# Optimization experiments

Hardware: AMD Instinct MI355X
Metric: run time of the kernel (lower is better)

The kernel has to match this reference:

```python
import jax, jax.numpy as jnp
import numpy as np

B, S, D, H = 4, 2048, 512, 8
E = D // H  # d_head = 64

def setup_inputs() -> dict:
    key = jax.random.key(0)
    ks = jax.random.split(key, 10)
    s_in = (1.0 / np.sqrt(D))
    x  = jax.random.normal(ks[0], (B, S, D), dtype=jnp.float32)
    Wq = jax.random.normal(ks[1], (H, D, E), dtype=jnp.float32) * s_in
    bq = jax.random.normal(ks[2], (H, E), dtype=jnp.float32) * 0.01
    Wk = jax.random.normal(ks[3], (H, D, E), dtype=jnp.float32) * s_in
    bk = jax.random.normal(ks[4], (H, E), dtype=jnp.float32) * 0.01
    Wv = jax.random.normal(ks[5], (H, D, E), dtype=jnp.float32) * s_in
    bv = jax.random.normal(ks[6], (H, E), dtype=jnp.float32) * 0.01
    Wo = jax.random.normal(ks[7], (D, D), dtype=jnp.float32) * s_in
    bo = jax.random.normal(ks[8], (D,), dtype=jnp.float32) * 0.01
    return {"x": x, "Wq": Wq, "bq": bq, "Wk": Wk, "bk": bk,
            "Wv": Wv, "bv": bv, "Wo": Wo, "bo": bo}

def reference(x, Wq, bq, Wk, bk, Wv, bv, Wo, bo):
    B_, S_, D_ = x.shape
    # per-head projections (batched over head axis h)
    q = jnp.einsum('bsd,hde->bhse', x, Wq) + bq[None, :, None, :]
    k = jnp.einsum('bsd,hde->bhse', x, Wk) + bk[None, :, None, :]
    v = jnp.einsum('bsd,hde->bhse', x, Wv) + bv[None, :, None, :]
    # NOTE: original scales by d_model**-0.5 (full D), not d_head**-0.5
    scale = jnp.asarray(D_, x.dtype) ** -0.5
    scores = jnp.einsum('bhse,bhte->bhst', q, k) * scale  # [B,H,S,S]
    causal = jnp.tril(jnp.ones((S_, S_), dtype=bool))
    scores = jnp.where(causal[None, None], scores, -jnp.inf)
    attn = jax.nn.softmax(scores, axis=-1)
    out = jnp.einsum('bhst,bhte->bhse', attn, v)  # [B,H,S,E]
    # concat heads along feature dim (head-major), matching torch.cat
    out = out.transpose(0, 2, 1, 3).reshape(B_, S_, D_)
    return out @ Wo + bo  # final projection; dropout never applied in source
```

## Files before the change

kernel.cpp:

```cpp
#include <hip/hip_runtime.h>

typedef unsigned short u16;
typedef __bf16 bf16x8 __attribute__((ext_vector_type(8)));
typedef short s16x4 __attribute__((ext_vector_type(4)));
typedef short s16x8 __attribute__((ext_vector_type(8)));
typedef float f32x4 __attribute__((ext_vector_type(4)));

#define BB 4
#define SS 2048
#define DD 512
#define HH 8
#define EE 64
#define MM 8192
#define BHSE (BB*HH*SS*EE)

__device__ __forceinline__ float b2f(u16 u) {
    return __uint_as_float(((unsigned int)u) << 16);
}
__device__ __forceinline__ u16 f2b(float f) {
    unsigned int v = __float_as_uint(f);
    v += 0x7fffu + ((v >> 16) & 1u);
    return (u16)(v >> 16);
}
__device__ __forceinline__ float loadE(const void* p, size_t idx, int isbf16) {
    return isbf16 ? b2f(((const u16*)p)[idx]) : ((const float*)p)[idx];
}
__device__ __forceinline__ f32x4 mfma16x16x16_bf16(s16x4 a, s16x4 b, f32x4 c) {
    return __builtin_amdgcn_mfma_f32_16x16x16bf16_1k(a, b, c, 0, 0, 0);
}

__device__ __forceinline__ int detect_bf16(const u16* x) {
    int sane = 0;
    for (int i = 0; i < 128; ++i) {
        float a = fabsf(b2f(x[2 * i]));
        if (a == 0.f || (a > 1e-4f && a < 100.f)) ++sane;
    }
    return sane >= 96;
}

__global__ __launch_bounds__(256) void transpose_weights(
    const void* __restrict__ Wq, const void* __restrict__ Wk,
    const void* __restrict__ Wv, const void* __restrict__ Wo,
    const u16* __restrict__ xin,
    u16* __restrict__ WT, u16* __restrict__ WoT, int* __restrict__ flag)
{
    const int isbf16 = detect_bf16(xin);
    if (blockIdx.x == 0 && threadIdx.x == 0) *flag = isbf16;

    const int j = blockIdx.x;
    const int job = j >> 6;
    const int t = j & 63;
    const void* src; u16* dst; int src_ld, dst_ld;
    if (job < 3) {
        const void* W = (job == 0) ? Wq : ((job == 1) ? Wk : Wv);
        int h = t >> 3, kt = t & 7;
        size_t off = (size_t)h * DD * EE + (size_t)kt * 64 * EE;
        src = isbf16 ? (const void*)(((const u16*)W) + off)
                     : (const void*)(((const float*)W) + off);
        src_ld = EE;
        dst = WT + (size_t)job * 512 * 512 + (size_t)(h * 64) * 512 + kt * 64;
        dst_ld = 512;
    } else {
        int a = t >> 3, b = t & 7;
        size_t off = (size_t)(a * 64) * 512 + b * 64;
        src = isbf16 ? (const void*)(((const u16*)Wo) + off)
                     : (const void*)(((const float*)Wo) + off);
        src_ld = 512;
        dst = WoT + (size_t)(b * 64) * 512 + a * 64;
        dst_ld = 512;
    }
    __shared__ __align__(16) u16 Ts[64 * 72];
    const int tid = threadIdx.x;
#pragma unroll
    for (int it = 0; it < 2; ++it) {
        int idx = it * 256 + tid;
        int r = idx >> 3, c = (idx & 7) << 3;
#pragma unroll
        for (int k = 0; k < 8; ++k) {
            float v = loadE(src, (size_t)r * src_ld + c + k, isbf16);
            Ts[(c + k) * 72 + r] = f2b(v);
        }
    }
    __syncthreads();
#pragma unroll
    for (int it = 0; it < 2; ++it) {
        int idx = it * 256 + tid;
        int r = idx >> 3, c = (idx & 7) << 3;
        *(bf16x8*)(dst + (size_t)r * dst_ld + c) = *(const bf16x8*)&Ts[r * 72 + c];
    }
}

__global__ __launch_bounds__(256) void gemm_qkv(
    const void* __restrict__ X, const u16* __restrict__ WT,
    const void* __restrict__ bq, const void* __restrict__ bk,
    const void* __restrict__ bv, u16* __restrict__ qkv,
    const int* __restrict__ flag)
{
    const float SCALE = 0.04419417382415922f;
    const int isbf16 = *flag;
    const int m0 = blockIdx.x * 64;
    const int n0 = blockIdx.y * 64;
    const int tid = threadIdx.x;
    const int wave = tid >> 6, lane = tid & 63;
    const int lq = lane & 15, quad = lane >> 4;
    __shared__ __align__(16) u16 As[64 * 72];
    __shared__ __align__(16) u16 Bs[64 * 72];
    f32x4 acc[4] = {};
    for (int k0 = 0; k0 < 512; k0 += 64) {
        __syncthreads();
#pragma unroll
        for (int it = 0; it < 2; ++it) {
            int idx = it * 256 + tid;
            int r = idx >> 3, c = (idx & 7) << 3;
            size_t eoff = (size_t)(m0 + r) * 512 + k0 + c;
            if (isbf16) {
                *(bf16x8*)&As[r * 72 + c] = *(const bf16x8*)(((const u16*)X) + eoff);
            } else {
                const float* Xf = ((const float*)X) + eoff;
                float4 f0 = *(const float4*)Xf;
                float4 f1 = *(const float4*)(Xf + 4);
                u16 tmp[8] = { f2b(f0.x), f2b(f0.y), f2b(f0.z), f2b(f0.w),
                               f2b(f1.x), f2b(f1.y), f2b(f1.z), f2b(f1.w) };
                *(bf16x8*)&As[r * 72 + c] = *(const bf16x8*)tmp;
            }
            *(bf16x8*)&Bs[r * 72 + c] = *(const bf16x8*)(WT + (size_t)(n0 + r) * 512 + k0 + c);
        }
        __syncthreads();
        const u16* Arow = &As[(16 * wave + lq) * 72];
        bf16x8 a0 = *(const bf16x8*)(Arow + quad * 8);
        bf16x8 a1 = *(const bf16x8*)(Arow + 32 + quad * 8);
#pragma unroll
        for (int nt = 0; nt < 4; ++nt) {
            const u16* Brow = &Bs[(nt * 16 + lq) * 72];
            bf16x8 b0 = *(const bf16x8*)(Brow + quad * 8);
            bf16x8 b1 = *(const bf16x8*)(Brow + 32 + quad * 8);
            acc[nt] = __builtin_amdgcn_mfma_f32_16x16x32_bf16(a0, b0, acc[nt], 0, 0, 0);
            acc[nt] = __builtin_amdgcn_mfma_f32_16x16x32_bf16(a1, b1, acc[nt], 0, 0, 0);
        }
    }
#pragma unroll
    for (int nt = 0; nt < 4; ++nt) {
#pragma unroll
        for (int r = 0; r < 4; ++r) {
            int m = m0 + 16 * wave + quad * 4 + r;
            int n = n0 + nt * 16 + lq;
            int proj = n >> 9, nn = n & 511;
            const void* bias = (proj == 0) ? bq : ((proj == 1) ? bk : bv);
            float v = acc[nt][r] + loadE(bias, nn, isbf16);
            if (proj == 0) v *= SCALE;
            int b = m >> 11, s = m & 2047, h = nn >> 6, e = nn & 63;
            qkv[(size_t)proj * BHSE + (((size_t)(b * HH + h) * SS + s) * EE + e)] = f2b(v);
        }
    }
}

struct Stage { uint4 k0, k1, va, vb; };

__device__ __forceinline__ void stage_load(Stage& st, const u16* Kh, const u16* Vh,
                                           int t0, int tid) {
    int r = tid >> 3, c = (tid & 7) * 8;
    st.k0 = *(const uint4*)(Kh + (size_t)(t0 + r) * 64 + c);
    st.k1 = *(const uint4*)(Kh + (size_t)(t0 + r + 32) * 64 + c);
    int t2 = 2 * (tid & 31), e8 = (tid >> 5) * 8;
    st.va = *(const uint4*)(Vh + (size_t)(t0 + t2) * 64 + e8);
    st.vb = *(const uint4*)(Vh + (size_t)(t0 + t2 + 1) * 64 + e8);
}
__device__ __forceinline__ void stage_write(const Stage& st, u16* Ksb, u16* VTsb, int tid) {
    int r = tid >> 3, c = (tid & 7) * 8;
    *(uint4*)(Ksb + r * 72 + c) = st.k0;
    *(uint4*)(Ksb + (r + 32) * 72 + c) = st.k1;
    int t2 = 2 * (tid & 31), e8 = (tid >> 5) * 8;
    int g2 = ((t2 >> 2) & 3) * 16 + ((t2 >> 4) << 2) + (t2 & 3);
    const unsigned* pa = (const unsigned*)&st.va;
    const unsigned* pb = (const unsigned*)&st.vb;
#pragma unroll
    for (int k = 0; k < 4; ++k) {
        unsigned lo = __builtin_amdgcn_perm(pb[k], pa[k], 0x05040100u);
        unsigned hi = __builtin_amdgcn_perm(pb[k], pa[k], 0x07060302u);
        *(unsigned*)(VTsb + (e8 + 2 * k) * 72 + g2) = lo;
        *(unsigned*)(VTsb + (e8 + 2 * k + 1) * 72 + g2) = hi;
    }
}

__device__ __forceinline__ void attn_tile(const u16* Ksb, const u16* VTsb,
    bf16x8 qf0, bf16x8 qf1, int lq, int quad, int wave, bool diag,
    f32x4 Ot[4], float& lacc)
{
#pragma unroll
    for (int half = 0; half < 2; ++half) {
        s16x4 vf[4][2];
#pragma unroll
        for (int et = 0; et < 4; ++et) {
            const u16* Vp = VTsb + (et * 16 + lq) * 72 + quad * 16 + half * 8;
            s16x8 v = *(const s16x8*)Vp;
            vf[et][0] = __builtin_shufflevector(v, v, 0, 1, 2, 3);
            vf[et][1] = __builtin_shufflevector(v, v, 4, 5, 6, 7);
        }
#pragma unroll
        for (int tj = 0; tj < 2; ++tj) {
            const int tt = half * 2 + tj;
            const u16* Krow = Ksb + (tt * 16 + lq) * 72;
            bf16x8 k0 = *(const bf16x8*)(Krow + quad * 8);
            bf16x8 k1 = *(const bf16x8*)(Krow + 32 + quad * 8);
            f32x4 sc = {};
            sc = __builtin_amdgcn_mfma_f32_16x16x32_bf16(k0, qf0, sc, 0, 0, 0);
            sc = __builtin_amdgcn_mfma_f32_16x16x32_bf16(k1, qf1, sc, 0, 0, 0);
            unsigned pu[4];
#pragma unroll
            for (int r = 0; r < 4; ++r) {
                float p = __expf(sc[r]);
                if (diag) {
                    int tl = tt * 16 + quad * 4 + r;
                    int ql = 16 * wave + lq;
                    p = (tl <= ql) ? p : 0.f;
                }
                lacc += __uint_as_float(__float_as_uint(p) & 0xffff0000u);
                pu[r] = __float_as_uint(p);
            }
            union { unsigned u[2]; s16x4 s; } pf;
            pf.u[0] = __builtin_amdgcn_perm(pu[1], pu[0], 0x07060302u);
            pf.u[1] = __builtin_amdgcn_perm(pu[3], pu[2], 0x07060302u);
#pragma unroll
            for (int et = 0; et < 4; ++et)
                Ot[et] = mfma16x16x16_bf16(vf[et][tj], pf.s, Ot[et]);
        }
    }
}

__global__ __launch_bounds__(256) void attn_kernel(
    const u16* __restrict__ Qg, const u16* __restrict__ Kg,
    const u16* __restrict__ Vg, u16* __restrict__ Og)
{
    const int bh = blockIdx.x;
    const int qb = ((int)gridDim.y - 1 - (int)blockIdx.y) * 64;
    const int nt = qb >> 6;
    const int tid = threadIdx.x;
    const int wave = tid >> 6, lane = tid & 63;
    const int lq = lane & 15, quad = lane >> 4;
    const int b = bh >> 3, h = bh & 7;

    const size_t base = (size_t)bh * SS * EE;
    const u16* Kh = Kg + base;
    const u16* Vh = Vg + base;

    __shared__ __align__(16) u16 Ks[2][64 * 72];
    __shared__ __align__(16) u16 VTs[2][64 * 72];

    const int qrow = qb + 16 * wave + lq;
    const u16* Qp = Qg + base + (size_t)qrow * EE;
    bf16x8 qf0 = *(const bf16x8*)(Qp + quad * 8);
    bf16x8 qf1 = *(const bf16x8*)(Qp + 32 + quad * 8);

    f32x4 Ot[4] = {};
    float lacc = 0.f;

    Stage st;
    stage_load(st, Kh, Vh, 0, tid);
    stage_write(st, Ks[0], VTs[0], tid);
    for (int i = 0; i <= nt; ++i) {
        __syncthreads();
        const int cur = i & 1;
        const bool more = (i < nt);
        if (more) stage_load(st, Kh, Vh, (i + 1) * 64, tid);
        attn_tile(Ks[cur], VTs[cur], qf0, qf1, lq, quad, wave, i == nt, Ot, lacc);
        if (more) stage_write(st, Ks[cur ^ 1], VTs[cur ^ 1], tid);
    }

    lacc += __shfl_xor(lacc, 16);
    lacc += __shfl_xor(lacc, 32);
    const float inv = 1.f / lacc;

    u16* Op = Og + (((size_t)(b * SS + qrow)) * HH + h) * EE;
#pragma unroll
    for (int et = 0; et < 4; ++et) {
        u16 tmp[4];
#pragma unroll
        for (int r = 0; r < 4; ++r) tmp[r] = f2b(Ot[et][r] * inv);
        *(uint2*)(Op + et * 16 + quad * 4) = *(const uint2*)tmp;
    }
}

__global__ __launch_bounds__(256) void gemm_out(
    const u16* __restrict__ A, const u16* __restrict__ WoT,
    const void* __restrict__ bo, void* __restrict__ out,
    const int* __restrict__ flag)
{
    const int isbf16 = *flag;
    const int m0 = blockIdx.x * 64;
    const int n0 = blockIdx.y * 64;
    const int tid = threadIdx.x;
    const int wave = tid >> 6, lane = tid & 63;
    const int lq = lane & 15, quad = lane >> 4;
    __shared__ __align__(16) u16 As[64 * 72];
    __shared__ __align__(16) u16 Bs[64 * 72];
    f32x4 acc[4] = {};
    for (int k0 = 0; k0 < 512; k0 += 64) {
        __syncthreads();
#pragma unroll
        for (int it = 0; it < 2; ++it) {
            int idx = it * 256 + tid;
            int r = idx >> 3, c = (idx & 7) << 3;
            *(bf16x8*)&As[r * 72 + c] = *(const bf16x8*)(A   + (size_t)(m0 + r) * 512 + k0 + c);
            *(bf16x8*)&Bs[r * 72 + c] = *(const bf16x8*)(WoT + (size_t)(n0 + r) * 512 + k0 + c);
        }
        __syncthreads();
        const u16* Arow = &As[(16 * wave + lq) * 72];
        bf16x8 a0 = *(const bf16x8*)(Arow + quad * 8);
        bf16x8 a1 = *(const bf16x8*)(Arow + 32 + quad * 8);
#pragma unroll
        for (int nt = 0; nt < 4; ++nt) {
            const u16* Brow = &Bs[(nt * 16 + lq) * 72];
            bf16x8 b0 = *(const bf16x8*)(Brow + quad * 8);
            bf16x8 b1 = *(const bf16x8*)(Brow + 32 + quad * 8);
            acc[nt] = __builtin_amdgcn_mfma_f32_16x16x32_bf16(a0, b0, acc[nt], 0, 0, 0);
            acc[nt] = __builtin_amdgcn_mfma_f32_16x16x32_bf16(a1, b1, acc[nt], 0, 0, 0);
        }
    }
#pragma unroll
    for (int nt = 0; nt < 4; ++nt) {
#pragma unroll
        for (int r = 0; r < 4; ++r) {
            int m = m0 + 16 * wave + quad * 4 + r;
            int n = n0 + nt * 16 + lq;
            float v = acc[nt][r] + loadE(bo, n, isbf16);
            if (isbf16) ((u16*)out)[(size_t)m * 512 + n] = f2b(v);
            else        ((float*)out)[(size_t)m * 512 + n] = v;
        }
    }
}

extern "C" void kernel_launch(void* const* d_in, const int* in_sizes, int n_in,
                              void* d_out, int out_size, void* d_ws, size_t ws_size,
                              hipStream_t stream) {
    const void* x  = d_in[0];
    const void* Wq = d_in[1];
    const void* bq = d_in[2];
    const void* Wk = d_in[3];
    const void* bk = d_in[4];
    const void* Wv = d_in[5];
    const void* bv = d_in[6];
    const void* Wo = d_in[7];
    const void* bo = d_in[8];

    u16* WT   = (u16*)d_ws;
    u16* WoT  = WT + 3 * 512 * 512;
    u16* qkv  = WoT + 512 * 512;
    u16* attn = qkv + 3 * (size_t)BHSE;
    int* flag = (int*)(attn + (size_t)BHSE);

    transpose_weights<<<256, 256, 0, stream>>>(Wq, Wk, Wv, Wo, (const u16*)x, WT, WoT, flag);
    gemm_qkv<<<dim3(MM / 64, 1536 / 64), 256, 0, stream>>>(x, WT, bq, bk, bv, qkv, flag);
    attn_kernel<<<dim3(BB * HH, SS / 64), 256, 0, stream>>>(qkv, qkv + BHSE, qkv + 2 * (size_t)BHSE, attn);
    gemm_out<<<dim3(MM / 64, 512 / 64), 256, 0, stream>>>(attn, WoT, bo, d_out, flag);
}
```

Before: 206.6 us.

## Enlarge GEMM tiles, use direct global-to-LDS loads with XOR swizzle

Both projection GEMMs now use larger block tiles (128x128 for QKV, 128x64 for output), with each wave computing a 64x64 or 64x32 sub-tile, so more MFMA work is done per LDS load. The bf16 paths stage tiles through global_load_lds, which writes straight into LDS without passing through registers, and use an XOR-swizzled unpadded layout to avoid LDS bank conflicts. The fp32 path keeps register staging but uses the same swizzled layout. The risk is fewer blocks, which can under-fill the GPU, plus higher register pressure from the larger accumulator tiles.

```diff
diff --git a/kernel.cpp b/kernel.cpp
--- a/kernel.cpp
+++ b/kernel.cpp
@@ -14,6 +14,9 @@
 #define MM 8192
 #define BHSE (BB*HH*SS*EE)
 
+#define GLOBAL_AS __attribute__((address_space(1)))
+#define LDS_AS    __attribute__((address_space(3)))
+
 __device__ __forceinline__ float b2f(u16 u) {
     return __uint_as_float(((unsigned int)u) << 16);
 }
@@ -27,6 +30,9 @@
 }
 __device__ __forceinline__ f32x4 mfma16x16x16_bf16(s16x4 a, s16x4 b, f32x4 c) {
     return __builtin_amdgcn_mfma_f32_16x16x16bf16_1k(a, b, c, 0, 0, 0);
+}
+__device__ __forceinline__ void load_lds16(const u16* g, u16* l) {
+    __builtin_amdgcn_global_load_lds((GLOBAL_AS void*)g, (LDS_AS void*)l, 16, 0, 0);
 }
 
 __device__ __forceinline__ int detect_bf16(const u16* x) {
@@ -90,6 +96,30 @@
     }
 }
 
+template<int MT, int NT>
+__device__ __forceinline__ void mfma_step(const u16* As, const u16* Bs,
+    int mh, int nh, int lq, int quad, f32x4 acc[MT][NT])
+{
+    const int sw = lq & 7;
+#pragma unroll
+    for (int kw = 0; kw < 2; ++kw) {
+        const int G = kw * 4 + quad;
+        const int col = ((G ^ sw) << 3);
+        bf16x8 a[MT], b[NT];
+#pragma unroll
+        for (int mt = 0; mt < MT; ++mt)
+            a[mt] = *(const bf16x8*)&As[(mh + mt * 16 + lq) * 64 + col];
+#pragma unroll
+        for (int nt = 0; nt < NT; ++nt)
+            b[nt] = *(const bf16x8*)&Bs[(nh + nt * 16 + lq) * 64 + col];
+#pragma unroll
+        for (int mt = 0; mt < MT; ++mt)
+#pragma unroll
+            for (int nt = 0; nt < NT; ++nt)
+                acc[mt][nt] = __builtin_amdgcn_mfma_f32_16x16x32_bf16(a[mt], b[nt], acc[mt][nt], 0, 0, 0);
+    }
+}
+
 __global__ __launch_bounds__(256) void gemm_qkv(
     const void* __restrict__ X, const u16* __restrict__ WT,
     const void* __restrict__ bq, const void* __restrict__ bk,
@@ -98,58 +128,69 @@
 {
     const float SCALE = 0.04419417382415922f;
     const int isbf16 = *flag;
-    const int m0 = blockIdx.x * 64;
-    const int n0 = blockIdx.y * 64;
+    const int m0 = blockIdx.x * 128;
+    const int n0 = blockIdx.y * 128;
     const int tid = threadIdx.x;
     const int wave = tid >> 6, lane = tid & 63;
     const int lq = lane & 15, quad = lane >> 4;
-    __shared__ __align__(16) u16 As[64 * 72];
-    __shared__ __align__(16) u16 Bs[64 * 72];
-    f32x4 acc[4] = {};
-    for (int k0 = 0; k0 < 512; k0 += 64) {
-        __syncthreads();
-#pragma unroll
-        for (int it = 0; it < 2; ++it) {
-            int idx = it * 256 + tid;
-            int r = idx >> 3, c = (idx & 7) << 3;
-            size_t eoff = (size_t)(m0 + r) * 512 + k0 + c;
-            if (isbf16) {
-                *(bf16x8*)&As[r * 72 + c] = *(const bf16x8*)(((const u16*)X) + eoff);
-            } else {
-                const float* Xf = ((const float*)X) + eoff;
-                float4 f0 = *(const float4*)Xf;
-                float4 f1 = *(const float4*)(Xf + 4);
-                u16 tmp[8] = { f2b(f0.x), f2b(f0.y), f2b(f0.z), f2b(f0.w),
-                               f2b(f1.x), f2b(f1.y), f2b(f1.z), f2b(f1.w) };
-                *(bf16x8*)&As[r * 72 + c] = *(const bf16x8*)tmp;
-            }
-            *(bf16x8*)&Bs[r * 72 + c] = *(const bf16x8*)(WT + (size_t)(n0 + r) * 512 + k0 + c);
-        }
-        __syncthreads();
-        const u16* Arow = &As[(16 * wave + lq) * 72];
-        bf16x8 a0 = *(const bf16x8*)(Arow + quad * 8);
-        bf16x8 a1 = *(const bf16x8*)(Arow + 32 + quad * 8);
+    const int mh = (wave & 1) * 64, nh = (wave >> 1) * 64;
+    __shared__ __align__(16) u16 As[128 * 64];
+    __shared__ __align__(16) u16 Bs[128 * 64];
+    f32x4 acc[4][4] = {};
+
+    const int swz = (lane & 7) ^ ((lane >> 3) & 7);
+    const size_t lane_off = (size_t)(lane >> 3) * 512 + 8 * swz;
+
+    if (isbf16) {
+        const u16* Xb = (const u16*)X;
+        for (int k0 = 0; k0 < 512; k0 += 64) {
+            __syncthreads();
+#pragma unroll
+            for (int jj = 0; jj < 4; ++jj) {
+                const int c = wave * 4 + jj;
+                load_lds16(Xb + (size_t)(m0 + 8 * c) * 512 + k0 + lane_off, &As[c * 512]);
+                load_lds16(WT + (size_t)(n0 + 8 * c) * 512 + k0 + lane_off, &Bs[c * 512]);
+            }
+            __syncthreads();
+            mfma_step<4, 4>(As, Bs, mh, nh, lq, quad, acc);
+        }
+    } else {
+        const float* Xf = (const float*)X;
+        for (int k0 = 0; k0 < 512; k0 += 64) {
+            __syncthreads();
+#pragma unroll
+            for (int it = 0; it < 4; ++it) {
+                int idx = it * 256 + tid;
+                int r = idx >> 3, cg = idx & 7;
+                const float* xp = Xf + (size_t)(m0 + r) * 512 + k0 + cg * 8;
+                u16 tmp[8];
+#pragma unroll
+                for (int k = 0; k < 8; ++k) tmp[k] = f2b(xp[k]);
+                *(bf16x8*)&As[r * 64 + (((cg) ^ (r & 7)) << 3)] = *(const bf16x8*)tmp;
+                *(bf16x8*)&Bs[r * 64 + (((cg) ^ (r & 7)) << 3)] =
+                    *(const bf16x8*)(WT + (size_t)(n0 + r) * 512 + k0 + cg * 8);
+            }
+            __syncthreads();
+            mfma_step<4, 4>(As, Bs, mh, nh, lq, quad, acc);
+        }
+    }
+
+    const int proj = n0 >> 9;
+    const void* bias = (proj == 0) ? bq : ((proj == 1) ? bk : bv);
+#pragma unroll
+    for (int mt = 0; mt < 4; ++mt) {
 #pragma unroll
         for (int nt = 0; nt < 4; ++nt) {
-            const u16* Brow = &Bs[(nt * 16 + lq) * 72];
-            bf16x8 b0 = *(const bf16x8*)(Brow + quad * 8);
-            bf16x8 b1 = *(const bf16x8*)(Brow + 32 + quad * 8);
-            acc[nt] = __builtin_amdgcn_mfma_f32_16x16x32_bf16(a0, b0, acc[nt], 0, 0, 0);
-            acc[nt] = __builtin_amdgcn_mfma_f32_16x16x32_bf16(a1, b1, acc[nt], 0, 0, 0);
-        }
-    }
-#pragma unroll
-    for (int nt = 0; nt < 4; ++nt) {
-#pragma unroll
-        for (int r = 0; r < 4; ++r) {
-            int m = m0 + 16 * wave + quad * 4 + r;
-            int n = n0 + nt * 16 + lq;
-            int proj = n >> 9, nn = n & 511;
-            const void* bias = (proj == 0) ? bq : ((proj == 1) ? bk : bv);
-            float v = acc[nt][r] + loadE(bias, nn, isbf16);
-            if (proj == 0) v *= SCALE;
-            int b = m >> 11, s = m & 2047, h = nn >> 6, e = nn & 63;
-            qkv[(size_t)proj * BHSE + (((size_t)(b * HH + h) * SS + s) * EE + e)] = f2b(v);
+#pragma unroll
+            for (int r = 0; r < 4; ++r) {
+                int m = m0 + mh + mt * 16 + quad * 4 + r;
+                int n = n0 + nh + nt * 16 + lq;
+                int nn = n & 511;
+                float v = acc[mt][nt][r] + loadE(bias, nn, isbf16);
+                if (proj == 0) v *= SCALE;
+                int b_ = m >> 11, s = m & 2047, h = nn >> 6, e = nn & 63;
+                qkv[(size_t)proj * BHSE + (((size_t)(b_ * HH + h) * SS + s) * EE + e)] = f2b(v);
+            }
         }
     }
 }
@@ -286,45 +327,46 @@
     const int* __restrict__ flag)
 {
     const int isbf16 = *flag;
-    const int m0 = blockIdx.x * 64;
+    const int m0 = blockIdx.x * 128;
     const int n0 = blockIdx.y * 64;
     const int tid = threadIdx.x;
     const int wave = tid >> 6, lane = tid & 63;
     const int lq = lane & 15, quad = lane >> 4;
-    __shared__ __align__(16) u16 As[64 * 72];
-    __shared__ __align__(16) u16 Bs[64 * 72];
-    f32x4 acc[4] = {};
+    const int mh = (wave & 1) * 64, nh = (wave >> 1) * 32;
+    __shared__ __align__(16) u16 As[128 * 64];
+    __shared__ __align__(16) u16 Bs[64 * 64];
+    f32x4 acc[4][2] = {};
+
+    const int swz = (lane & 7) ^ ((lane >> 3) & 7);
+    const size_t lane_off = (size_t)(lane >> 3) * 512 + 8 * swz;
+
     for (int k0 = 0; k0 < 512; k0 += 64) {
         __syncthreads();
 #pragma unroll
-        for (int it = 0; it < 2; ++it) {
-            int idx = it * 256 + tid;
-            int r = idx >> 3, c = (idx & 7) << 3;
-            *(bf16x8*)&As[r * 72 + c] = *(const bf16x8*)(A   + (size_t)(m0 + r) * 512 + k0 + c);
-            *(bf16x8*)&Bs[r * 72 + c] = *(const bf16x8*)(WoT + (size_t)(n0 + r) * 512 + k0 + c);
+        for (int jj = 0; jj < 4; ++jj) {
+            const int c = wave * 4 + jj;
+            load_lds16(A + (size_t)(m0 + 8 * c) * 512 + k0 + lane_off, &As[c * 512]);
+        }
+#pragma unroll
+        for (int jj = 0; jj < 2; ++jj) {
+            const int c = wave * 2 + jj;
+            load_lds16(WoT + (size_t)(n0 + 8 * c) * 512 + k0 + lane_off, &Bs[c * 512]);
         }
         __syncthreads();
-        const u16* Arow = &As[(16 * wave + lq) * 72];
-        bf16x8 a0 = *(const bf16x8*)(Arow + quad * 8);
-        bf16x8 a1 = *(const bf16x8*)(Arow + 32 + quad * 8);
-#pragma unroll
-        for (int nt = 0; nt < 4; ++nt) {
-            const u16* Brow = &Bs[(nt * 16 + lq) * 72];
-            bf16x8 b0 = *(const bf16x8*)(Brow + quad * 8);
-            bf16x8 b1 = *(const bf16x8*)(Brow + 32 + quad * 8);
-            acc[nt] = __builtin_amdgcn_mfma_f32_16x16x32_bf16(a0, b0, acc[nt], 0, 0, 0);
-            acc[nt] = __builtin_amdgcn_mfma_f32_16x16x32_bf16(a1, b1, acc[nt], 0, 0, 0);
-        }
-    }
-#pragma unroll
-    for (int nt = 0; nt < 4; ++nt) {
-#pragma unroll
-        for (int r = 0; r < 4; ++r) {
-            int m = m0 + 16 * wave + quad * 4 + r;
-            int n = n0 + nt * 16 + lq;
-            float v = acc[nt][r] + loadE(bo, n, isbf16);
-            if (isbf16) ((u16*)out)[(size_t)m * 512 + n] = f2b(v);
-            else        ((float*)out)[(size_t)m * 512 + n] = v;
+        mfma_step<4, 2>(As, Bs, mh, nh, lq, quad, acc);
+    }
+#pragma unroll
+    for (int mt = 0; mt < 4; ++mt) {
+#pragma unroll
+        for (int nt = 0; nt < 2; ++nt) {
+#pragma unroll
+            for (int r = 0; r < 4; ++r) {
+                int m = m0 + mh + mt * 16 + quad * 4 + r;
+                int n = n0 + nh + nt * 16 + lq;
+                float v = acc[mt][nt][r] + loadE(bo, n, isbf16);
+                if (isbf16) ((u16*)out)[(size_t)m * 512 + n] = f2b(v);
+                else        ((float*)out)[(size_t)m * 512 + n] = v;
+            }
         }
     }
 }
@@ -349,7 +391,7 @@
     int* flag = (int*)(attn + (size_t)BHSE);
 
     transpose_weights<<<256, 256, 0, stream>>>(Wq, Wk, Wv, Wo, (const u16*)x, WT, WoT, flag);
-    gemm_qkv<<<dim3(MM / 64, 1536 / 64), 256, 0, stream>>>(x, WT, bq, bk, bv, qkv, flag);
+    gemm_qkv<<<dim3(MM / 128, 1536 / 128), 256, 0, stream>>>(x, WT, bq, bk, bv, qkv, flag);
     attn_kernel<<<dim3(BB * HH, SS / 64), 256, 0, stream>>>(qkv, qkv + BHSE, qkv + 2 * (size_t)BHSE, attn);
-    gemm_out<<<dim3(MM / 64, 512 / 64), 256, 0, stream>>>(attn, WoT, bo, d_out, flag);
-}
+    gemm_out<<<dim3(MM / 128, 512 / 64), 256, 0, stream>>>(attn, WoT, bo, d_out, flag);
+}
```

Result: slower. 212.4 us (+2.8%).
